# Optimization experiments

Hardware: AMD Instinct MI355X
Metric: run time of the kernel (lower is better)

## Reference

```python
import jax, jax.numpy as jnp
import numpy as np

B, N, C = 1, 50000, 128
E, D = 800000, 2


def setup_inputs() -> dict:
    key = jax.random.key(0)
    k1, k2, k3 = jax.random.split(key, 3)
    x = jax.random.normal(k1, (B, N, C), dtype=jnp.float32)
    edge_weights = jax.random.normal(k2, (B, E, D), dtype=jnp.float32)
    directed_edges = jax.random.randint(k3, (B, E, 2), 0, N, dtype=jnp.int64)
    return {"x": x, "edge_weights": edge_weights, "directed_edges": directed_edges}


def reference(x, edge_weights, directed_edges):
    # x: [B, N, C] node features; edge_weights: [B, E, D]; directed_edges: [B, E, 2] = (target, source)
    b, n, c = x.shape
    _, e, d = edge_weights.shape
    target = directed_edges[..., 0]  # [B, E]
    source = directed_edges[..., 1]  # [B, E]
    bidx = jnp.arange(b)[:, None]  # [B, 1] broadcasts against [B, E]
    # gather node diffs per edge: [B, E, C]
    diff = x[bidx, source] - x[bidx, target]
    # weight by edge direction vector and flatten (C, D) -> C*D, matching torch reshape order
    message = jnp.einsum('bed,bec->becd', edge_weights, diff).reshape(b, e, c * d)
    # scatter-add into per-node gradient accumulator: [B, N, C*D]
    out = jnp.zeros((b, n, c * d), dtype=message.dtype)
    out = out.at[bidx, target].add(message)
    return out
```

## Files before the change

### kernel.cpp

```cpp
#include <hip/hip_runtime.h>


#define CAP 32
#define OVF_CAP 65536
#define NPART 8

typedef unsigned short u16;
typedef unsigned int u32;

__device__ __forceinline__ u16 f2bf(float f) {
  u32 u = __float_as_uint(f);
  return (u16)((u + 0x7FFFu + ((u >> 16) & 1u)) >> 16);
}
__device__ __forceinline__ float bf2f(u16 v) {
  return __uint_as_float(((u32)v) << 16);
}

__global__ __launch_bounds__(256) void k_cvt(const float* __restrict__ x,
                                             u16* __restrict__ xb, int total4) {
  const int stride = gridDim.x * blockDim.x;
  for (int i = blockIdx.x * blockDim.x + threadIdx.x; i < total4; i += stride) {
    const float4 v = reinterpret_cast<const float4*>(x)[i];
    ushort4 o;
    o.x = f2bf(v.x); o.y = f2bf(v.y); o.z = f2bf(v.z); o.w = f2bf(v.w);
    reinterpret_cast<ushort4*>(xb)[i] = o;
  }
}

__device__ __forceinline__ void append_one(int tgt, int src, float wx, float wy,
                                           int* counts, int4* rec,
                                           int* ovfcnt, int4* ovflist) {
  const int pos = atomicAdd(&counts[tgt], 1);
  if (pos < CAP) {
    int4 r;
    r.x = src; r.y = __float_as_int(wx); r.z = __float_as_int(wy); r.w = 0;
    rec[(size_t)tgt * CAP + pos] = r;
  } else {
    const int op = atomicAdd(ovfcnt, 1);
    if (op < OVF_CAP) {
      int4 r;
      r.x = tgt; r.y = src; r.z = __float_as_int(wx); r.w = __float_as_int(wy);
      ovflist[op] = r;
    }
  }
}

__global__ __launch_bounds__(256) void k_append_p(const int* __restrict__ edges,
                                                  const float* __restrict__ ew,
                                                  int* __restrict__ counts,
                                                  int4* __restrict__ rec,
                                                  int* __restrict__ ovfcnt,
                                                  int4* __restrict__ ovflist,
                                                  int E, int N) {
  const int part = blockIdx.x & (NPART - 1);
  const int bidx = blockIdx.x >> 3;
  const int nblk = gridDim.x >> 3;
  const int lo = (int)((long long)part * N / NPART);
  const int hi = (int)((long long)(part + 1) * N / NPART);
  const int npairs = E >> 1;
  const int stride = nblk * blockDim.x;

  for (int i = bidx * blockDim.x + threadIdx.x; i < npairs; i += stride) {
    const int4 p = reinterpret_cast<const int4*>(edges)[i];
    const bool in0 = (p.x >= lo) & (p.x < hi);
    const bool in1 = (p.z >= lo) & (p.z < hi);
    if (in0 | in1) {
      const float4 w = reinterpret_cast<const float4*>(ew)[i];
      if (in0) append_one(p.x, p.y, w.x, w.y, counts, rec, ovfcnt, ovflist);
      if (in1) append_one(p.z, p.w, w.z, w.w, counts, rec, ovfcnt, ovflist);
    }
  }
  if (E & 1) {
    const int e = E - 1;
    if (bidx == 0 && threadIdx.x == 0) {
      const int t = edges[2 * e];
      if (t >= lo && t < hi) {
        const float2 w = reinterpret_cast<const float2*>(ew)[e];
        append_one(t, edges[2 * e + 1], w.x, w.y, counts, rec, ovfcnt, ovflist);
      }
    }
  }
}

#define ACC8(X0, X1, X2, X3, WX, WY)                    \
  a0 = fmaf((WX), (X0), a0); a1 = fmaf((WY), (X0), a1); \
  a2 = fmaf((WX), (X1), a2); a3 = fmaf((WY), (X1), a3); \
  a4 = fmaf((WX), (X2), a4); a5 = fmaf((WY), (X2), a5); \
  a6 = fmaf((WX), (X3), a6); a7 = fmaf((WY), (X3), a7);

__global__ __launch_bounds__(256) void k_gather4(const float* __restrict__ x,
                                                 const u16* __restrict__ xb,
                                                 const int* __restrict__ counts,
                                                 const int4* __restrict__ rec,
                                                 float* __restrict__ out, int n) {
  const int lane = threadIdx.x & 63;
  const int node = (blockIdx.x * blockDim.x + threadIdx.x) >> 6;
  if (node >= n) return;
  const int c = lane & 31;
  const int half = lane >> 5;

  const int deg = min(counts[node], CAP);

  const float4 xt = *reinterpret_cast<const float4*>(x + (size_t)node * 128 + 4 * c);

  int rsrc = 0;
  float rwx = 0.f, rwy = 0.f;
  if (deg > 0) {
    const int li = min(lane, deg - 1);
    const int4 r = rec[(size_t)node * CAP + li];
    rsrc = r.x;
    if (lane < deg) { rwx = __int_as_float(r.y); rwy = __int_as_float(r.z); }
  }

  float a0 = 0.f, a1 = 0.f, a2 = 0.f, a3 = 0.f;
  float a4 = 0.f, a5 = 0.f, a6 = 0.f, a7 = 0.f;

  const int npair = (deg + 1) >> 1;
  int i = 0;
  for (; i + 4 <= npair; i += 4) {
    const int j0 = 2 * i + half;
    const int s0 = __shfl(rsrc, j0);
    const int s1 = __shfl(rsrc, j0 + 2);
    const int s2 = __shfl(rsrc, j0 + 4);
    const int s3 = __shfl(rsrc, j0 + 6);
    const ushort4 u0 = *reinterpret_cast<const ushort4*>(xb + (size_t)s0 * 128 + 4 * c);
    const ushort4 u1 = *reinterpret_cast<const ushort4*>(xb + (size_t)s1 * 128 + 4 * c);
    const ushort4 u2 = *reinterpret_cast<const ushort4*>(xb + (size_t)s2 * 128 + 4 * c);
    const ushort4 u3 = *reinterpret_cast<const ushort4*>(xb + (size_t)s3 * 128 + 4 * c);
    const float w0x = __shfl(rwx, j0),     w0y = __shfl(rwy, j0);
    const float w1x = __shfl(rwx, j0 + 2), w1y = __shfl(rwy, j0 + 2);
    const float w2x = __shfl(rwx, j0 + 4), w2y = __shfl(rwy, j0 + 4);
    const float w3x = __shfl(rwx, j0 + 6), w3y = __shfl(rwy, j0 + 6);
    ACC8(bf2f(u0.x), bf2f(u0.y), bf2f(u0.z), bf2f(u0.w), w0x, w0y)
    ACC8(bf2f(u1.x), bf2f(u1.y), bf2f(u1.z), bf2f(u1.w), w1x, w1y)
    ACC8(bf2f(u2.x), bf2f(u2.y), bf2f(u2.z), bf2f(u2.w), w2x, w2y)
    ACC8(bf2f(u3.x), bf2f(u3.y), bf2f(u3.z), bf2f(u3.w), w3x, w3y)
  }
  for (; i < npair; ++i) {
    const int j = 2 * i + half;
    const int s0 = __shfl(rsrc, j);
    const ushort4 u0 = *reinterpret_cast<const ushort4*>(xb + (size_t)s0 * 128 + 4 * c);
    const float w0x = __shfl(rwx, j), w0y = __shfl(rwy, j);
    ACC8(bf2f(u0.x), bf2f(u0.y), bf2f(u0.z), bf2f(u0.w), w0x, w0y)
  }

  float swx = rwx, swy = rwy;
  for (int off = 1; off < 64; off <<= 1) {
    swx += __shfl_xor(swx, off);
    swy += __shfl_xor(swy, off);
  }

  a0 += __shfl_xor(a0, 32); a1 += __shfl_xor(a1, 32);
  a2 += __shfl_xor(a2, 32); a3 += __shfl_xor(a3, 32);
  a4 += __shfl_xor(a4, 32); a5 += __shfl_xor(a5, 32);
  a6 += __shfl_xor(a6, 32); a7 += __shfl_xor(a7, 32);

  float4 o;
  if (half == 0) {
    o.x = a0 - swx * xt.x; o.y = a1 - swy * xt.x;
    o.z = a2 - swx * xt.y; o.w = a3 - swy * xt.y;
  } else {
    o.x = a4 - swx * xt.z; o.y = a5 - swy * xt.z;
    o.z = a6 - swx * xt.w; o.w = a7 - swy * xt.w;
  }
  *reinterpret_cast<float4*>(out + (size_t)node * 256 + 8 * c + 4 * half) = o;
}

__global__ __launch_bounds__(256) void k_overflow(const float* __restrict__ x,
                                                  const int* __restrict__ ovfcnt,
                                                  const int4* __restrict__ ovflist,
                                                  float* __restrict__ out) {
  const int lane = threadIdx.x & 63;
  const int wave = (blockIdx.x * blockDim.x + threadIdx.x) >> 6;
  const int nwaves = (gridDim.x * blockDim.x) >> 6;
  const int novf = min(*ovfcnt, OVF_CAP);
  for (int i = wave; i < novf; i += nwaves) {
    const int4 r = ovflist[i];
    const int tgt = r.x, src = r.y;
    const float wx = __int_as_float(r.z), wy = __int_as_float(r.w);
    const float2 vs = *reinterpret_cast<const float2*>(x + (size_t)src * 128 + 2 * lane);
    const float2 vt = *reinterpret_cast<const float2*>(x + (size_t)tgt * 128 + 2 * lane);
    const float d0 = vs.x - vt.x;
    const float d1 = vs.y - vt.y;
    float* o = out + (size_t)tgt * 256 + 4 * lane;
    unsafeAtomicAdd(o + 0, wx * d0);
    unsafeAtomicAdd(o + 1, wy * d0);
    unsafeAtomicAdd(o + 2, wx * d1);
    unsafeAtomicAdd(o + 3, wy * d1);
  }
}

#define CAPF 64
__global__ __launch_bounds__(256) void k_append_f(const int* __restrict__ edges,
                                                  const float2* __restrict__ ew,
                                                  int* __restrict__ counts,
                                                  int4* __restrict__ rec, int E) {
  const int e = blockIdx.x * blockDim.x + threadIdx.x;
  if (e >= E) return;
  const int2 ts = reinterpret_cast<const int2*>(edges)[e];
  const float2 w = ew[e];
  const int pos = atomicAdd(&counts[ts.x], 1);
  if (pos < CAPF) {
    int4 r;
    r.x = ts.y; r.y = __float_as_int(w.x); r.z = __float_as_int(w.y); r.w = 0;
    rec[(size_t)ts.x * CAPF + pos] = r;
  }
}

#define ACCF(X, WX, WY)                                   \
  a0 = fmaf((WX), (X).x, a0); a1 = fmaf((WY), (X).x, a1); \
  a2 = fmaf((WX), (X).y, a2); a3 = fmaf((WY), (X).y, a3); \
  a4 = fmaf((WX), (X).z, a4); a5 = fmaf((WY), (X).z, a5); \
  a6 = fmaf((WX), (X).w, a6); a7 = fmaf((WY), (X).w, a7);

__global__ __launch_bounds__(256) void k_gather3(const float* __restrict__ x,
                                                 const int* __restrict__ counts,
                                                 const int4* __restrict__ rec,
                                                 float* __restrict__ out, int n) {
  const int lane = threadIdx.x & 63;
  const int node = (blockIdx.x * blockDim.x + threadIdx.x) >> 6;
  if (node >= n) return;
  const int c = lane & 31;
  const int half = lane >> 5;
  const int deg = min(counts[node], CAPF);
  const float4 xt = *reinterpret_cast<const float4*>(x + (size_t)node * 128 + 4 * c);
  int rsrc = 0; float rwx = 0.f, rwy = 0.f;
  if (deg > 0) {
    const int li = min(lane, deg - 1);
    const int4 r = rec[(size_t)node * CAPF + li];
    rsrc = r.x;
    if (lane < deg) { rwx = __int_as_float(r.y); rwy = __int_as_float(r.z); }
  }
  float a0 = 0.f, a1 = 0.f, a2 = 0.f, a3 = 0.f;
  float a4 = 0.f, a5 = 0.f, a6 = 0.f, a7 = 0.f;
  const int npair = (deg + 1) >> 1;
  for (int i = 0; i < npair; ++i) {
    const int j = 2 * i + half;
    const int s0 = __shfl(rsrc, j);
    const float4 X = *reinterpret_cast<const float4*>(x + (size_t)s0 * 128 + 4 * c);
    const float wx = __shfl(rwx, j), wy = __shfl(rwy, j);
    ACCF(X, wx, wy)
  }
  float swx = rwx, swy = rwy;
  for (int off = 1; off < 64; off <<= 1) {
    swx += __shfl_xor(swx, off);
    swy += __shfl_xor(swy, off);
  }
  a0 += __shfl_xor(a0, 32); a1 += __shfl_xor(a1, 32);
  a2 += __shfl_xor(a2, 32); a3 += __shfl_xor(a3, 32);
  a4 += __shfl_xor(a4, 32); a5 += __shfl_xor(a5, 32);
  a6 += __shfl_xor(a6, 32); a7 += __shfl_xor(a7, 32);
  float4 o;
  if (half == 0) {
    o.x = a0 - swx * xt.x; o.y = a1 - swy * xt.x;
    o.z = a2 - swx * xt.y; o.w = a3 - swy * xt.y;
  } else {
    o.x = a4 - swx * xt.z; o.y = a5 - swy * xt.z;
    o.z = a6 - swx * xt.w; o.w = a7 - swy * xt.w;
  }
  *reinterpret_cast<float4*>(out + (size_t)node * 256 + 8 * c + 4 * half) = o;
}

__global__ __launch_bounds__(256) void k_atomic(const float* __restrict__ x,
                                                const float* __restrict__ ew,
                                                const int* __restrict__ edges,
                                                float* __restrict__ out, int E) {
  const int lane = threadIdx.x & 63;
  const int wave = (blockIdx.x * blockDim.x + threadIdx.x) >> 6;
  const int nwaves = (gridDim.x * blockDim.x) >> 6;
  for (int e = wave; e < E; e += nwaves) {
    const int2 ts = *reinterpret_cast<const int2*>(edges + 2ll * e);
    const float2 w = *reinterpret_cast<const float2*>(ew + 2ll * e);
    const float2 vs = *reinterpret_cast<const float2*>(x + (size_t)ts.y * 128 + 2 * lane);
    const float2 vt = *reinterpret_cast<const float2*>(x + (size_t)ts.x * 128 + 2 * lane);
    const float d0 = vs.x - vt.x;
    const float d1 = vs.y - vt.y;
    float* o = out + (size_t)ts.x * 256 + 4 * lane;
    unsafeAtomicAdd(o + 0, w.x * d0);
    unsafeAtomicAdd(o + 1, w.y * d0);
    unsafeAtomicAdd(o + 2, w.x * d1);
    unsafeAtomicAdd(o + 3, w.y * d1);
  }
}

extern "C" void kernel_launch(void* const* d_in, const int* in_sizes, int n_in,
                              void* d_out, int out_size, void* d_ws, size_t ws_size,
                              hipStream_t stream) {
  const float* x = (const float*)d_in[0];
  const float* ewf = (const float*)d_in[1];
  const int* edges = (const int*)d_in[2];
  float* out = (float*)d_out;
  const float2* ew = (const float2*)ewf;

  const int E = in_sizes[1] / 2;
  const int N = in_sizes[0] / 128;

  size_t cnt_sec = ((size_t)(N + 1) * 4 + 255) & ~(size_t)255;
  size_t xb_sec = ((size_t)N * 128 * 2 + 255) & ~(size_t)255;
  size_t rec_sec = (size_t)N * CAP * 16;
  size_t need_bf16 = cnt_sec + xb_sec + rec_sec + (size_t)OVF_CAP * 16;
  size_t need_f32 = cnt_sec + (size_t)N * CAPF * 16;

  char* wsb = (char*)d_ws;

  if (ws_size >= need_bf16 && (E & 1) == 0) {
    int* counts = (int*)wsb;
    int* ovfcnt = counts + N;
    u16* xb = (u16*)(wsb + cnt_sec);
    int4* rec = (int4*)(wsb + cnt_sec + xb_sec);
    int4* ovflist = (int4*)(wsb + cnt_sec + xb_sec + rec_sec);
    hipMemsetAsync(counts, 0, (size_t)(N + 1) * 4, stream);
    k_append_p<<<3328, 256, 0, stream>>>(edges, ewf, counts, rec, ovfcnt, ovflist, E, N);
    k_cvt<<<2048, 256, 0, stream>>>(x, xb, N * 128 / 4);
    k_gather4<<<(N * 64 + 255) / 256, 256, 0, stream>>>(x, xb, counts, rec, out, N);
    k_overflow<<<32, 256, 0, stream>>>(x, ovfcnt, ovflist, out);
    return;
  }

  if (ws_size >= need_f32) {
    int* counts = (int*)wsb;
    int4* rec = (int4*)(wsb + cnt_sec);
    hipMemsetAsync(counts, 0, (size_t)N * 4, stream);
    k_append_f<<<(E + 255) / 256, 256, 0, stream>>>(edges, ew, counts, rec, E);
    k_gather3<<<(N * 64 + 255) / 256, 256, 0, stream>>>(x, counts, rec, out, N);
    return;
  }

  hipMemsetAsync(d_out, 0, (size_t)out_size * sizeof(float), stream);
  k_atomic<<<2048, 256, 0, stream>>>(x, ewf, edges, out, E);
}
```

Baseline: 100.7 us.

## Fuse bf16 conversion into append kernel and fold overflow handling into gather

Merges the edge-append and x-to-bf16 conversion kernels into one launch, with separate block ranges doing each job. Overflow edges are now handled inside the gather kernel by nodes whose count exceeds the cap, which scan the overflow list, so the separate atomic overflow kernel is gone. 64-bit index math is replaced with 32-bit shifts, guarded by an N bound. This cuts launch overhead and lets the two independent prep phases overlap. The cost is a linear scan of the overflow list per high-degree node, which could be expensive when many nodes overflow.

```diff
diff --git a/kernel.cpp b/kernel.cpp
--- a/kernel.cpp
+++ b/kernel.cpp
@@ -4,6 +4,7 @@
 #define CAP 32
 #define OVF_CAP 65536
 #define NPART 8
+#define NAPP 3328
 
 typedef unsigned short u16;
 typedef unsigned int u32;
@@ -14,17 +15,6 @@
 }
 __device__ __forceinline__ float bf2f(u16 v) {
   return __uint_as_float(((u32)v) << 16);
-}
-
-__global__ __launch_bounds__(256) void k_cvt(const float* __restrict__ x,
-                                             u16* __restrict__ xb, int total4) {
-  const int stride = gridDim.x * blockDim.x;
-  for (int i = blockIdx.x * blockDim.x + threadIdx.x; i < total4; i += stride) {
-    const float4 v = reinterpret_cast<const float4*>(x)[i];
-    ushort4 o;
-    o.x = f2bf(v.x); o.y = f2bf(v.y); o.z = f2bf(v.z); o.w = f2bf(v.w);
-    reinterpret_cast<ushort4*>(xb)[i] = o;
-  }
 }
 
 __device__ __forceinline__ void append_one(int tgt, int src, float wx, float wy,
@@ -34,7 +24,7 @@
   if (pos < CAP) {
     int4 r;
     r.x = src; r.y = __float_as_int(wx); r.z = __float_as_int(wy); r.w = 0;
-    rec[(size_t)tgt * CAP + pos] = r;
+    rec[tgt * CAP + pos] = r;
   } else {
     const int op = atomicAdd(ovfcnt, 1);
     if (op < OVF_CAP) {
@@ -45,39 +35,42 @@
   }
 }
 
-__global__ __launch_bounds__(256) void k_append_p(const int* __restrict__ edges,
-                                                  const float* __restrict__ ew,
-                                                  int* __restrict__ counts,
-                                                  int4* __restrict__ rec,
-                                                  int* __restrict__ ovfcnt,
-                                                  int4* __restrict__ ovflist,
-                                                  int E, int N) {
-  const int part = blockIdx.x & (NPART - 1);
-  const int bidx = blockIdx.x >> 3;
-  const int nblk = gridDim.x >> 3;
-  const int lo = (int)((long long)part * N / NPART);
-  const int hi = (int)((long long)(part + 1) * N / NPART);
-  const int npairs = E >> 1;
-  const int stride = nblk * blockDim.x;
-
-  for (int i = bidx * blockDim.x + threadIdx.x; i < npairs; i += stride) {
-    const int4 p = reinterpret_cast<const int4*>(edges)[i];
-    const bool in0 = (p.x >= lo) & (p.x < hi);
-    const bool in1 = (p.z >= lo) & (p.z < hi);
-    if (in0 | in1) {
-      const float4 w = reinterpret_cast<const float4*>(ew)[i];
-      if (in0) append_one(p.x, p.y, w.x, w.y, counts, rec, ovfcnt, ovflist);
-      if (in1) append_one(p.z, p.w, w.z, w.w, counts, rec, ovfcnt, ovflist);
+__global__ __launch_bounds__(256) void k_prep(const int* __restrict__ edges,
+                                              const float* __restrict__ ew,
+                                              const float* __restrict__ x,
+                                              int* __restrict__ counts,
+                                              int4* __restrict__ rec,
+                                              int* __restrict__ ovfcnt,
+                                              int4* __restrict__ ovflist,
+                                              u16* __restrict__ xb,
+                                              int E, int N, int total4) {
+  if (blockIdx.x < NAPP) {
+    const int part = blockIdx.x & (NPART - 1);
+    const int bidx = blockIdx.x >> 3;
+    const int nblk = NAPP >> 3;
+    const int lo = (int)((long long)part * N / NPART);
+    const int hi = (int)((long long)(part + 1) * N / NPART);
+    const int npairs = E >> 1;
+    const int stride = nblk * blockDim.x;
+    for (int i = bidx * blockDim.x + threadIdx.x; i < npairs; i += stride) {
+      const int4 p = reinterpret_cast<const int4*>(edges)[i];
+      const bool in0 = (p.x >= lo) & (p.x < hi);
+      const bool in1 = (p.z >= lo) & (p.z < hi);
+      if (in0 | in1) {
+        const float4 w = reinterpret_cast<const float4*>(ew)[i];
+        if (in0) append_one(p.x, p.y, w.x, w.y, counts, rec, ovfcnt, ovflist);
+        if (in1) append_one(p.z, p.w, w.z, w.w, counts, rec, ovfcnt, ovflist);
+      }
     }
-  }
-  if (E & 1) {
-    const int e = E - 1;
-    if (bidx == 0 && threadIdx.x == 0) {
-      const int t = edges[2 * e];
-      if (t >= lo && t < hi) {
-        const float2 w = reinterpret_cast<const float2*>(ew)[e];
-        append_one(t, edges[2 * e + 1], w.x, w.y, counts, rec, ovfcnt, ovflist);
-      }
+  } else {
+    const int nb = gridDim.x - NAPP;
+    const int stride = nb * blockDim.x;
+    for (int i = (blockIdx.x - NAPP) * blockDim.x + threadIdx.x; i < total4;
+         i += stride) {
+      const float4 v = reinterpret_cast<const float4*>(x)[i];
+      ushort4 o;
+      o.x = f2bf(v.x); o.y = f2bf(v.y); o.z = f2bf(v.z); o.w = f2bf(v.w);
+      reinterpret_cast<ushort4*>(xb)[i] = o;
     }
   }
 }
@@ -88,26 +81,30 @@
   a4 = fmaf((WX), (X2), a4); a5 = fmaf((WY), (X2), a5); \
   a6 = fmaf((WX), (X3), a6); a7 = fmaf((WY), (X3), a7);
 
-__global__ __launch_bounds__(256) void k_gather4(const float* __restrict__ x,
+__global__ __launch_bounds__(256) void k_gather5(const float* __restrict__ x,
                                                  const u16* __restrict__ xb,
                                                  const int* __restrict__ counts,
                                                  const int4* __restrict__ rec,
+                                                 const int* __restrict__ ovfcnt,
+                                                 const int4* __restrict__ ovflist,
                                                  float* __restrict__ out, int n) {
   const int lane = threadIdx.x & 63;
   const int node = (blockIdx.x * blockDim.x + threadIdx.x) >> 6;
   if (node >= n) return;
   const int c = lane & 31;
   const int half = lane >> 5;
-
-  const int deg = min(counts[node], CAP);
-
-  const float4 xt = *reinterpret_cast<const float4*>(x + (size_t)node * 128 + 4 * c);
+  const int c4 = 4 * c;
+
+  const int cnt = counts[node];
+  const int deg = min(cnt, CAP);
+
+  const float4 xt = *reinterpret_cast<const float4*>(x + (node << 7) + c4);
 
   int rsrc = 0;
   float rwx = 0.f, rwy = 0.f;
   if (deg > 0) {
     const int li = min(lane, deg - 1);
-    const int4 r = rec[(size_t)node * CAP + li];
+    const int4 r = rec[(node << 5) + li];
     rsrc = r.x;
     if (lane < deg) { rwx = __int_as_float(r.y); rwy = __int_as_float(r.z); }
   }
@@ -123,10 +120,10 @@
     const int s1 = __shfl(rsrc, j0 + 2);
     const int s2 = __shfl(rsrc, j0 + 4);
     const int s3 = __shfl(rsrc, j0 + 6);
-    const ushort4 u0 = *reinterpret_cast<const ushort4*>(xb + (size_t)s0 * 128 + 4 * c);
-    const ushort4 u1 = *reinterpret_cast<const ushort4*>(xb + (size_t)s1 * 128 + 4 * c);
-    const ushort4 u2 = *reinterpret_cast<const ushort4*>(xb + (size_t)s2 * 128 + 4 * c);
-    const ushort4 u3 = *reinterpret_cast<const ushort4*>(xb + (size_t)s3 * 128 + 4 * c);
+    const ushort4 u0 = *reinterpret_cast<const ushort4*>(xb + (s0 << 7) + c4);
+    const ushort4 u1 = *reinterpret_cast<const ushort4*>(xb + (s1 << 7) + c4);
+    const ushort4 u2 = *reinterpret_cast<const ushort4*>(xb + (s2 << 7) + c4);
+    const ushort4 u3 = *reinterpret_cast<const ushort4*>(xb + (s3 << 7) + c4);
     const float w0x = __shfl(rwx, j0),     w0y = __shfl(rwy, j0);
     const float w1x = __shfl(rwx, j0 + 2), w1y = __shfl(rwy, j0 + 2);
     const float w2x = __shfl(rwx, j0 + 4), w2y = __shfl(rwy, j0 + 4);
@@ -139,7 +136,7 @@
   for (; i < npair; ++i) {
     const int j = 2 * i + half;
     const int s0 = __shfl(rsrc, j);
-    const ushort4 u0 = *reinterpret_cast<const ushort4*>(xb + (size_t)s0 * 128 + 4 * c);
+    const ushort4 u0 = *reinterpret_cast<const ushort4*>(xb + (s0 << 7) + c4);
     const float w0x = __shfl(rwx, j), w0y = __shfl(rwy, j);
     ACC8(bf2f(u0.x), bf2f(u0.y), bf2f(u0.z), bf2f(u0.w), w0x, w0y)
   }
@@ -154,6 +151,25 @@
   a2 += __shfl_xor(a2, 32); a3 += __shfl_xor(a3, 32);
   a4 += __shfl_xor(a4, 32); a5 += __shfl_xor(a5, 32);
   a6 += __shfl_xor(a6, 32); a7 += __shfl_xor(a7, 32);
+
+  if (cnt > CAP) {
+    const int novf = min(*ovfcnt, OVF_CAP);
+    for (int k = 0; k < novf; ++k) {
+      const int4 r = ovflist[k];
+      if (r.x == node) {
+        const float wx = __int_as_float(r.z), wy = __int_as_float(r.w);
+        const float4 X = *reinterpret_cast<const float4*>(x + (r.y << 7) + c4);
+        if (half == 0) {
+          a0 = fmaf(wx, X.x, a0); a1 = fmaf(wy, X.x, a1);
+          a2 = fmaf(wx, X.y, a2); a3 = fmaf(wy, X.y, a3);
+        } else {
+          a4 = fmaf(wx, X.z, a4); a5 = fmaf(wy, X.z, a5);
+          a6 = fmaf(wx, X.w, a6); a7 = fmaf(wy, X.w, a7);
+        }
+        swx += wx; swy += wy;
+      }
+    }
+  }
 
   float4 o;
   if (half == 0) {
@@ -163,31 +179,7 @@
     o.x = a4 - swx * xt.z; o.y = a5 - swy * xt.z;
     o.z = a6 - swx * xt.w; o.w = a7 - swy * xt.w;
   }
-  *reinterpret_cast<float4*>(out + (size_t)node * 256 + 8 * c + 4 * half) = o;
-}
-
-__global__ __launch_bounds__(256) void k_overflow(const float* __restrict__ x,
-                                                  const int* __restrict__ ovfcnt,
-                                                  const int4* __restrict__ ovflist,
-                                                  float* __restrict__ out) {
-  const int lane = threadIdx.x & 63;
-  const int wave = (blockIdx.x * blockDim.x + threadIdx.x) >> 6;
-  const int nwaves = (gridDim.x * blockDim.x) >> 6;
-  const int novf = min(*ovfcnt, OVF_CAP);
-  for (int i = wave; i < novf; i += nwaves) {
-    const int4 r = ovflist[i];
-    const int tgt = r.x, src = r.y;
-    const float wx = __int_as_float(r.z), wy = __int_as_float(r.w);
-    const float2 vs = *reinterpret_cast<const float2*>(x + (size_t)src * 128 + 2 * lane);
-    const float2 vt = *reinterpret_cast<const float2*>(x + (size_t)tgt * 128 + 2 * lane);
-    const float d0 = vs.x - vt.x;
-    const float d1 = vs.y - vt.y;
-    float* o = out + (size_t)tgt * 256 + 4 * lane;
-    unsafeAtomicAdd(o + 0, wx * d0);
-    unsafeAtomicAdd(o + 1, wy * d0);
-    unsafeAtomicAdd(o + 2, wx * d1);
-    unsafeAtomicAdd(o + 3, wy * d1);
-  }
+  *reinterpret_cast<float4*>(out + (node << 8) + 8 * c + 4 * half) = o;
 }
 
 #define CAPF 64
@@ -303,17 +295,17 @@
 
   char* wsb = (char*)d_ws;
 
-  if (ws_size >= need_bf16 && (E & 1) == 0) {
+  if (ws_size >= need_bf16 && (E & 1) == 0 && N <= 4000000) {
     int* counts = (int*)wsb;
     int* ovfcnt = counts + N;
     u16* xb = (u16*)(wsb + cnt_sec);
     int4* rec = (int4*)(wsb + cnt_sec + xb_sec);
     int4* ovflist = (int4*)(wsb + cnt_sec + xb_sec + rec_sec);
     hipMemsetAsync(counts, 0, (size_t)(N + 1) * 4, stream);
-    k_append_p<<<3328, 256, 0, stream>>>(edges, ewf, counts, rec, ovfcnt, ovflist, E, N);
-    k_cvt<<<2048, 256, 0, stream>>>(x, xb, N * 128 / 4);
-    k_gather4<<<(N * 64 + 255) / 256, 256, 0, stream>>>(x, xb, counts, rec, out, N);
-    k_overflow<<<32, 256, 0, stream>>>(x, ovfcnt, ovflist, out);
+    k_prep<<<NAPP + 1024, 256, 0, stream>>>(edges, ewf, x, counts, rec, ovfcnt,
+                                            ovflist, xb, E, N, N * 128 / 4);
+    k_gather5<<<(N * 64 + 255) / 256, 256, 0, stream>>>(x, xb, counts, rec,
+                                                        ovfcnt, ovflist, out, N);
     return;
   }
 
```

Result: faster. 96.56 us (-4.1%).
